# Optimization experiments

Hardware: AMD Instinct MI355X
Metric: run time of the kernel (lower is better)

## Reference

```python
import jax, jax.numpy as jnp
import numpy as np

V = 100000   # char_size
E = 256      # embedding_dim
H = 512      # hidden_dim
Hh = H // 2  # per-direction hidden
L = 20       # label_size
T = 4096     # sequence length
START = 18
STOP = 19
NEG = -10000.0


def setup_inputs() -> dict:
    key = jax.random.key(0)
    ks = jax.random.split(key, 16)
    s = 0.05
    x = jax.random.randint(ks[0], (1, T), 0, V, dtype=jnp.int32)
    emb = jax.random.normal(ks[1], (V, E), jnp.float32) * s
    w_ih_f = jax.random.normal(ks[2], (4 * Hh, E), jnp.float32) * s
    w_hh_f = jax.random.normal(ks[3], (4 * Hh, Hh), jnp.float32) * s
    b_ih_f = jax.random.normal(ks[4], (4 * Hh,), jnp.float32) * s
    b_hh_f = jax.random.normal(ks[5], (4 * Hh,), jnp.float32) * s
    w_ih_b = jax.random.normal(ks[6], (4 * Hh, E), jnp.float32) * s
    w_hh_b = jax.random.normal(ks[7], (4 * Hh, Hh), jnp.float32) * s
    b_ih_b = jax.random.normal(ks[8], (4 * Hh,), jnp.float32) * s
    b_hh_b = jax.random.normal(ks[9], (4 * Hh,), jnp.float32) * s
    w_out = jax.random.normal(ks[10], (L, H), jnp.float32) * s
    b_out = jax.random.normal(ks[11], (L,), jnp.float32) * s
    transitions = jax.random.normal(ks[12], (L, L), jnp.float32)
    transitions = transitions.at[START, :].set(NEG).at[:, STOP].set(NEG)
    h0 = jax.random.normal(ks[13], (2, Hh), jnp.float32)  # [direction, Hh], batch=1
    c0 = jax.random.normal(ks[14], (2, Hh), jnp.float32)
    return {"x": x, "emb": emb,
            "w_ih_f": w_ih_f, "w_hh_f": w_hh_f, "b_ih_f": b_ih_f, "b_hh_f": b_hh_f,
            "w_ih_b": w_ih_b, "w_hh_b": w_hh_b, "b_ih_b": b_ih_b, "b_hh_b": b_hh_b,
            "w_out": w_out, "b_out": b_out, "transitions": transitions,
            "h0": h0, "c0": c0}


def _lstm_dir(xs, w_ih, w_hh, b_ih, b_hh, h0, c0, reverse):
    # xs: [T, E]; PyTorch gate order i, f, g, o
    def step(carry, x_t):
        h, c = carry
        z = x_t @ w_ih.T + b_ih + h @ w_hh.T + b_hh  # [4*Hh]
        i, f, g, o = jnp.split(z, 4)
        i = jax.nn.sigmoid(i); f = jax.nn.sigmoid(f); o = jax.nn.sigmoid(o)
        g = jnp.tanh(g)
        c = f * c + i * g
        h = o * jnp.tanh(c)
        return (h, c), h
    _, hs = jax.lax.scan(step, (h0, c0), xs, reverse=reverse)
    return hs  # [T, Hh]


def _viterbi(feats, transitions):
    # feats: [T, L]; transitions[to, from]
    alpha0 = jnp.full((L,), NEG, feats.dtype).at[START].set(0.0)
    trT = transitions.T  # [from, to]
    def step(alpha, frame):
        smat = alpha[:, None] + frame[None, :] + trT  # [from, to]
        return jnp.max(smat, axis=0), jnp.argmax(smat, axis=0)
    alpha, bptrs = jax.lax.scan(step, alpha0, feats)  # bptrs: [T, L]
    final = alpha + transitions[STOP, :]
    score = jnp.max(final)
    best_last = jnp.argmax(final)
    def back(tag, bp):
        prev = bp[tag]
        return prev, prev
    _, prevs = jax.lax.scan(back, best_last, bptrs[1:], reverse=True)  # [T-1]
    path = jnp.concatenate([prevs, best_last[None]])  # [T]
    return score, path


def reference(x, emb, w_ih_f, w_hh_f, b_ih_f, b_hh_f, w_ih_b, w_hh_b, b_ih_b, b_hh_b,
              w_out, b_out, transitions, h0, c0):
    xs = emb[x[0]]  # [T, E], batch = 1
    h_f = _lstm_dir(xs, w_ih_f, w_hh_f, b_ih_f, b_hh_f, h0[0], c0[0], reverse=False)
    h_b = _lstm_dir(xs, w_ih_b, w_hh_b, b_ih_b, b_hh_b, h0[1], c0[1], reverse=True)
    lstm_out = jnp.concatenate([h_f, h_b], axis=-1)  # [T, H]
    feats = lstm_out @ w_out.T + b_out  # [T, L]
    score, path = _viterbi(feats, transitions)
    return score, path
```

## Files before the change

kernel.cpp:

```cpp
#include <hip/hip_runtime.h>
#include <hip/hip_bf16.h>
#include <stdint.h>

#define TT 4096
#define EE 256
#define LL 20
#define STARTT 18
#define STOPP 19
#define NEGV -10000.0f
#define NCH 256

typedef short v8s __attribute__((ext_vector_type(8)));
typedef float v4f __attribute__((ext_vector_type(4)));
typedef int   v4i __attribute__((ext_vector_type(4)));

__device__ inline float bf2f(unsigned short u){
  unsigned int x = ((unsigned int)u) << 16;
  return __builtin_bit_cast(float, x);
}
__device__ inline unsigned short f2bf(float f){
  unsigned int x = __builtin_bit_cast(unsigned int, f);
  unsigned int r = (x + 0x7FFFu + ((x >> 16) & 1u)) >> 16;
  return (unsigned short)r;
}

#if __has_builtin(__builtin_amdgcn_sdot4)
#define SDOT4(a,b,c) __builtin_amdgcn_sdot4((int)(a),(int)(b),(c),false)
#else
__device__ inline int sdot4_sw(int a, int b, int c){
  return c + (int)(char)(a)        * (int)(char)(b)
           + (int)(char)(a >> 8)   * (int)(char)(b >> 8)
           + (int)(char)(a >> 16)  * (int)(char)(b >> 16)
           + (int)(char)(a >> 24)  * (int)(char)(b >> 24);
}
#define SDOT4(a,b,c) sdot4_sw((int)(a),(int)(b),(c))
#endif

#define BARRIER_LDS() asm volatile("s_waitcnt lgkmcnt(0)\ns_barrier" ::: "memory")

constexpr size_t OFF_U    = 0;
constexpr size_t SZ_U     = 2ull*TT*1024*2;
constexpr size_t OFF_X    = OFF_U + SZ_U;
constexpr size_t SZ_X     = (size_t)TT*EE*2;
constexpr size_t OFF_WIH  = OFF_X + SZ_X;
constexpr size_t SZ_WIH   = 2048ull*256*2;
constexpr size_t OFF_BIAS = OFF_WIH + SZ_WIH;
constexpr size_t SZ_BIAS  = 2048ull*4;
constexpr size_t OFF_WQ   = OFF_BIAS + SZ_BIAS;
constexpr size_t SZ_WQ    = 2ull*8*8*4*64*16;
constexpr size_t OFF_WQD  = OFF_WQ + SZ_WQ;
constexpr size_t SZ_WQD   = 2ull*8*4*64*16;
constexpr size_t OFF_FS   = OFF_WQD + SZ_WQD;
constexpr size_t SZ_FS    = 2ull*256*16;
constexpr size_t OFF_WOP  = OFF_FS + SZ_FS;
constexpr size_t SZ_WOP   = 32ull*512*2;
constexpr size_t OFF_HOUT = OFF_WOP + SZ_WOP;
constexpr size_t SZ_HOUT  = (size_t)TT*512*2;
constexpr size_t OFF_FE   = OFF_HOUT + SZ_HOUT;
constexpr size_t SZ_FE    = (size_t)TT*LL*4;
constexpr size_t OFF_P    = OFF_FE + SZ_FE;
constexpr size_t SZ_P     = 256ull*400*4;
constexpr size_t OFF_BAL  = OFF_P + SZ_P;
constexpr size_t SZ_BAL   = 20736;
constexpr size_t OFF_BP   = OFF_BAL + SZ_BAL;
constexpr size_t SZ_BP    = (size_t)TT*LL;
constexpr size_t OFF_M    = OFF_BP + SZ_BP;
constexpr size_t SZ_M     = 256ull*LL;
constexpr size_t OFF_EG   = OFF_M + SZ_M + 64;


__global__ void k_gather(const int* __restrict__ x, const float* __restrict__ emb,
                         unsigned short* __restrict__ X){
  int t = blockIdx.x;
  int xt = x[t];
  const float4* src = (const float4*)(emb + (size_t)xt * EE);
  float4 v = src[threadIdx.x];
  ushort4 o;
  o.x = f2bf(v.x); o.y = f2bf(v.y); o.z = f2bf(v.z); o.w = f2bf(v.w);
  ((ushort4*)(X + (size_t)t * EE))[threadIdx.x] = o;
}

__global__ void k_wih(const float* __restrict__ wf, const float* __restrict__ wb,
                      unsigned short* __restrict__ WIH){
  int gid = blockIdx.x * 256 + threadIdx.x;
  int row = gid >> 5, c8 = gid & 31;
  const float* src = (row < 1024 ? wf + (size_t)row * EE : wb + (size_t)(row - 1024) * EE) + c8 * 8;
  unsigned short* dst = WIH + (size_t)row * 256 + c8 * 8;
#pragma unroll
  for (int i = 0; i < 8; i++) dst[i] = f2bf(src[i]);
}

__global__ void k_bias(const float* bf, const float* hf, const float* bb, const float* hb,
                       float* __restrict__ bias){
  int i = blockIdx.x * 256 + threadIdx.x;
  int r = i & 1023;
  bias[i] = (i < 1024) ? (bf[r] + hf[r]) : (bb[r] + hb[r]);
}

__global__ void k_wout(const float* __restrict__ wout, unsigned short* __restrict__ WOP){
  int gid = blockIdx.x * 256 + threadIdx.x;
  int row = gid >> 9, k = gid & 511;
  WOP[gid] = (row < LL) ? f2bf(wout[row * 512 + k]) : 0;
}

__global__ void k_whh9(const float* __restrict__ whf, const float* __restrict__ whb,
                       unsigned int* __restrict__ WQ, unsigned int* __restrict__ WQD,
                       float* __restrict__ FS){
  int row = blockIdx.x;
  int d = row >> 10, R = row & 1023;
  int g = R >> 8, J = R & 255;
  int w = J >> 5, tp = (J >> 4) & 1, n = J & 15;
  int nt = g * 2 + tp;
  const float* W = (d ? whb : whf) + (size_t)R * 256;
  int t = threadIdx.x;
  float4 v = ((const float4*)W)[t];
  float m = fmaxf(fmaxf(fabsf(v.x), fabsf(v.y)), fmaxf(fabsf(v.z), fabsf(v.w)));
#pragma unroll
  for (int o = 32; o >= 1; o >>= 1) m = fmaxf(m, __shfl_down(m, o));
  m = __shfl(m, 0);
  float sc = (m > 0.f) ? (m / 127.f) : 1.f;
  float inv = 1.f / sc;
  int a = (int)rintf(v.x * inv), b = (int)rintf(v.y * inv);
  int c = (int)rintf(v.z * inv), e4 = (int)rintf(v.w * inv);
  unsigned int pack = ((unsigned)a & 255u) | (((unsigned)b & 255u) << 8)
                    | (((unsigned)c & 255u) << 16) | (((unsigned)e4 & 255u) << 24);
  int kt = t >> 4, q = (t >> 2) & 3, comp = t & 3;
  int lane = q * 16 + n;
  if (nt == 7){
    size_t didx = (((size_t)d * 8 + w) * 4 + kt) * 64 + lane;
    WQD[didx * 4 + comp] = pack;
  } else {
    size_t widx = ((((size_t)d * 8 + w) * 8 + nt) * 4 + kt) * 64 + lane;
    WQ[widx * 4 + comp] = pack;
  }
  if (t == 0) FS[((size_t)d * 256 + J) * 4 + g] = sc;
}

__global__ void k_gemm_u(const unsigned short* __restrict__ X,
                         const unsigned short* __restrict__ WIH,
                         const float* __restrict__ bias,
                         unsigned short* __restrict__ U){
  int wave = threadIdx.x >> 6, l = threadIdx.x & 63;
  int tile = blockIdx.x * 4 + wave;
  int mt = tile & 255, nt = tile >> 8;
  int lm = l & 15, lq = l >> 4;
  const unsigned short* Arow = X   + (size_t)(mt * 16 + lm) * 256 + lq * 8;
  const unsigned short* Brow = WIH + (size_t)(nt * 16 + lm) * 256 + lq * 8;
  v4f acc = {0.f, 0.f, 0.f, 0.f};
#pragma unroll
  for (int kb = 0; kb < 8; kb++){
    v8s a = *(const v8s*)(Arow + kb * 32);
    v8s b = *(const v8s*)(Brow + kb * 32);
    acc = __builtin_amdgcn_mfma_f32_16x16x32_bf16(a, b, acc, 0, 0, 0);
  }
  int n = nt * 16 + lm;
  int dd = n >> 10, r = n & 1023;
  int g = r >> 8, J = r & 255;
  float bi = bias[n];
#pragma unroll
  for (int r4 = 0; r4 < 4; r4++){
    int t = mt * 16 + lq * 4 + r4;
    U[(((size_t)(dd * TT + t)) * 256 + J) * 4 + g] = f2bf(acc[r4] + bi);
  }
}


#define NT7(M) M(0) M(1) M(2) M(3) M(4) M(5) M(6)

#define DECLWB(nt) v4i wb0_##nt, wb1_##nt, wb2_##nt, wb3_##nt;
#define LOADWB(nt) { wb0_##nt = WQv[base + ((nt)*4 + 0) * 64]; \
                     wb1_##nt = WQv[base + ((nt)*4 + 1) * 64]; \
                     wb2_##nt = WQv[base + ((nt)*4 + 2) * 64]; \
                     wb3_##nt = WQv[base + ((nt)*4 + 3) * 64]; }
#define MF4(nt) \
  acc_##nt = __builtin_amdgcn_mfma_i32_16x16x64_i8(hA0, wb0_##nt, zero,     0, 0, 0); \
  acc_##nt = __builtin_amdgcn_mfma_i32_16x16x64_i8(hA1, wb1_##nt, acc_##nt, 0, 0, 0); \
  acc_##nt = __builtin_amdgcn_mfma_i32_16x16x64_i8(hA2, wb2_##nt, acc_##nt, 0, 0, 0); \
  acc_##nt = __builtin_amdgcn_mfma_i32_16x16x64_i8(hA3, wb3_##nt, acc_##nt, 0, 0, 0);

__global__ void __launch_bounds__(512)
__attribute__((amdgpu_waves_per_eu(2, 2)))
k_lstm13(
    const unsigned short* __restrict__ U, const v4i* __restrict__ WQv,
    const v4i* __restrict__ WQDv, const float4* __restrict__ FS4,
    const float* __restrict__ h0, const float* __restrict__ c0,
    unsigned short* __restrict__ hout){
  int d = blockIdx.x;
  int tid = threadIdx.x;
  int w = tid >> 6;
  int l = tid & 63;
  int q = l >> 4;
  int n = l & 15;
  int tp = l >> 5;
  int Jsel = w * 32 + tp * 16 + n;
  bool pub = ((l & 16) == 0);

  __shared__ __align__(16) unsigned char hb[2][256];

  NT7(DECLWB)
  v4i wd0, wd1, wd2, wd3;
  {
    size_t base = ((size_t)(d * 8 + w)) * 2048 + l;
    NT7(LOADWB)
    size_t dbase = ((size_t)(d * 8 + w)) * 256 + l;
    wd0 = WQDv[dbase];        wd1 = WQDv[dbase + 64];
    wd2 = WQDv[dbase + 128];  wd3 = WQDv[dbase + 192];
  }

  float4 fsv = FS4[(size_t)d * 256 + Jsel];
  float fs8x = fsv.x * (8.f/127.f), fs1x = fsv.x * (1.f/127.f);
  float fs8y = fsv.y * (8.f/127.f), fs1y = fsv.y * (1.f/127.f);
  float fs8z = fsv.z * (8.f/127.f), fs1z = fsv.z * (1.f/127.f);
  float fs8w = fsv.w * (8.f/127.f), fs1w = fsv.w * (1.f/127.f);

  float cst = c0[d * 256 + Jsel];
  if (pub){
    float hini = h0[d * 256 + Jsel];
    hini = fminf(fmaxf(hini, -8.f), 8.f);
    hb[0][Jsel] = (unsigned char)(char)(int)rintf(hini * (127.f / 8.f));
  }

  const unsigned short* Up0 = U + (size_t)d * TT * 1024 + (size_t)Jsel * 4;
  int stp = d ? -1 : 1;
  int tA = d ? TT - 1 : 0;
  uint2 u_c = *(const uint2*)(Up0 + (size_t)tA * 1024);
  uint2 u_n = *(const uint2*)(Up0 + (size_t)(tA + stp) * 1024);

  unsigned short* hp = hout + (size_t)tA * 512 + d * 256 + Jsel;

  v4i zero = {0, 0, 0, 0};

  __syncthreads();

  for (int s = 0; s < TT; s++){
    int par = s & 1;
    int tt = d ? (TT - 1 - s) : s;

    const char* hbase = (const char*)(&hb[par][0]) + (q << 4);
    v4i hA0 = *(const v4i*)(hbase);
    v4i hA1 = *(const v4i*)(hbase + 64);
    v4i hA2 = *(const v4i*)(hbase + 128);
    v4i hA3 = *(const v4i*)(hbase + 192);

    bool s0 = (s == 0);
    float fx = s0 ? fs8x : fs1x;
    float fy = s0 ? fs8y : fs1y;
    float fz = s0 ? fs8z : fs1z;
    float fw = s0 ? fs8w : fs1w;
    float u_i = bf2f((unsigned short)(u_c.x & 0xffffu));
    float u_f = bf2f((unsigned short)(u_c.x >> 16));
    float u_g = bf2f((unsigned short)(u_c.y & 0xffffu));
    float u_o = bf2f((unsigned short)(u_c.y >> 16));

    int ad = 0;
    ad = SDOT4(wd0.x, hA0.x, ad); ad = SDOT4(wd0.y, hA0.y, ad);
    ad = SDOT4(wd0.z, hA0.z, ad); ad = SDOT4(wd0.w, hA0.w, ad);
    ad = SDOT4(wd1.x, hA1.x, ad); ad = SDOT4(wd1.y, hA1.y, ad);
    ad = SDOT4(wd1.z, hA1.z, ad); ad = SDOT4(wd1.w, hA1.w, ad);
    ad = SDOT4(wd2.x, hA2.x, ad); ad = SDOT4(wd2.y, hA2.y, ad);
    ad = SDOT4(wd2.z, hA2.z, ad); ad = SDOT4(wd2.w, hA2.w, ad);
    ad = SDOT4(wd3.x, hA3.x, ad); ad = SDOT4(wd3.y, hA3.y, ad);
    ad = SDOT4(wd3.z, hA3.z, ad); ad = SDOT4(wd3.w, hA3.w, ad);
    ad += __shfl_xor(ad, 16);
    ad += __shfl_xor(ad, 32);

    v4i acc_0, acc_1, acc_2, acc_3, acc_4, acc_5, acc_6;
    MF4(0) MF4(1)
    int aI = tp ? acc_1[0] : acc_0[0];
    float zi = fmaf((float)aI, fx, u_i);
    float ea = __expf(-zi);
    float gi = __builtin_amdgcn_rcpf(1.f + ea);

    MF4(2) MF4(3)
    int aF = tp ? acc_3[0] : acc_2[0];
    float zf = fmaf((float)aF, fy, u_f);
    float eb = __expf(-zf);
    float gf = __builtin_amdgcn_rcpf(1.f + eb);

    MF4(4) MF4(5)
    int aG = tp ? acc_5[0] : acc_4[0];
    float zg = fmaf((float)aG, fz, u_g);
    float zc = fminf(fmaxf(zg, -20.f), 20.f);
    float ec = __expf(-2.f * zc);
    float gg = (1.f - ec) * __builtin_amdgcn_rcpf(1.f + ec);
    cst = fmaf(gf, cst, gi * gg);
    float cc = fminf(fmaxf(cst, -20.f), 20.f);
    float e2 = __expf(-2.f * cc);
    float th = (1.f - e2) * __builtin_amdgcn_rcpf(1.f + e2);

    MF4(6)
    int aO = tp ? ad : acc_6[0];
    float zo = fmaf((float)aO, fw, u_o);
    float ed = __expf(-zo);
    float go = __builtin_amdgcn_rcpf(1.f + ed);
    float h = go * th;

    u_c = u_n;
    {
      int t2 = tt + 2 * stp;
      t2 = t2 < 0 ? 0 : (t2 > TT - 1 ? TT - 1 : t2);
      u_n = *(const uint2*)(Up0 + (size_t)t2 * 1024);
    }

    if (pub){
      int qv = (int)rintf(h * 127.f);
      hb[par ^ 1][Jsel] = (unsigned char)(char)qv;
      *hp = f2bf(h);
    }
    hp += stp * 512;

    BARRIER_LDS();
  }
}

__global__ void k_feats2(const unsigned short* __restrict__ HOUT,
                         const unsigned short* __restrict__ WOP,
                         const float* __restrict__ bout,
                         float* __restrict__ feats){
  int wave = threadIdx.x >> 6, l = threadIdx.x & 63;
  int tile = blockIdx.x * 4 + wave;
  int mt = tile & 255, nt = tile >> 8;
  int lm = l & 15, lq = l >> 4;
  const unsigned short* Arow = HOUT + (size_t)(mt * 16 + lm) * 512 + lq * 8;
  const unsigned short* Brow = WOP  + (size_t)(nt * 16 + lm) * 512 + lq * 8;
  v4f acc = {0.f, 0.f, 0.f, 0.f};
#pragma unroll
  for (int kb = 0; kb < 16; kb++){
    v8s a = *(const v8s*)(Arow + kb * 32);
    v8s b = *(const v8s*)(Brow + kb * 32);
    acc = __builtin_amdgcn_mfma_f32_16x16x32_bf16(a, b, acc, 0, 0, 0);
  }
  int n = nt * 16 + lm;
  if (n < LL){
    float bi = bout[n];
#pragma unroll
    for (int r4 = 0; r4 < 4; r4++){
      int t = mt * 16 + lq * 4 + r4;
      feats[t * LL + n] = acc[r4] + bi;
    }
  }
}

__global__ void k_vchunk(const float* __restrict__ feats, const float* __restrict__ trans,
                         float* __restrict__ P){
  int c = blockIdx.x, j = threadIdx.x;
  __shared__ float Ps[2][LL][LL];
  bool act = j < LL;
  float trow[LL];
  if (act){
#pragma unroll
    for (int i = 0; i < LL; i++) trow[i] = trans[j * LL + i];
    for (int i = 0; i < LL; i++) Ps[0][i][j] = (i == j) ? 0.f : -1e30f;
  }
  __syncthreads();
  for (int s = 0; s < 16; s++){
    int t = c * 16 + s;
    int pb = s & 1;
    if (act){
      float fj = feats[t * LL + j];
      for (int i = 0; i < LL; i++){
        float m = Ps[pb][i][0] + trow[0];
#pragma unroll
        for (int mm = 1; mm < LL; mm++) m = fmaxf(m, Ps[pb][i][mm] + trow[mm]);
        Ps[pb ^ 1][i][j] = m + fj;
      }
    }
    __syncthreads();
  }
  if (act)
    for (int i = 0; i < LL; i++) P[((size_t)c * LL + i) * LL + j] = Ps[0][i][j];
}

__global__ void k_vscan(const float* __restrict__ P, float* __restrict__ bal){
  int tid = threadIdx.x;
  bool act = tid < LL;
  __shared__ float al[LL];
  __shared__ float Pl[400];
  if (act){
    float a = (tid == STARTT) ? 0.f : NEGV;
    al[tid] = a;
    bal[tid] = a;
  }
  for (int k = tid; k < 400; k += 64) Pl[k] = P[k];
  __syncthreads();
  for (int c = 0; c < NCH; c++){
    float p0 = 0.f, p1 = 0.f, p2 = 0.f, p3 = 0.f, p4 = 0.f, p5 = 0.f, p6 = 0.f;
    if (c + 1 < NCH){
      const float* Pn = P + (size_t)(c + 1) * 400;
      p0 = Pn[tid];        p1 = Pn[tid + 64];  p2 = Pn[tid + 128];
      p3 = Pn[tid + 192];  p4 = Pn[tid + 256]; p5 = Pn[tid + 320];
      if (tid + 384 < 400) p6 = Pn[tid + 384];
    }
    float m = -1e30f;
    if (act){
      m = al[0] + Pl[tid];
#pragma unroll
      for (int i = 1; i < LL; i++) m = fmaxf(m, al[i] + Pl[i * LL + tid]);
    }
    __syncthreads();
    if (act){
      al[tid] = m;
      bal[(c + 1) * LL + tid] = m;
    }
    if (c + 1 < NCH){
      Pl[tid] = p0;        Pl[tid + 64] = p1;  Pl[tid + 128] = p2;
      Pl[tid + 192] = p3;  Pl[tid + 256] = p4; Pl[tid + 320] = p5;
      if (tid + 384 < 400) Pl[tid + 384] = p6;
    }
    __syncthreads();
  }
}

__global__ void k_vbp(const float* __restrict__ feats, const float* __restrict__ trans,
                      const float* __restrict__ bal, unsigned char* __restrict__ bp,
                      unsigned char* __restrict__ M){
  int c = blockIdx.x, j = threadIdx.x;
  bool act = j < LL;
  __shared__ float al[2][LL];
  __shared__ unsigned char bpl[16][LL];
  float trow[LL];
  if (act){
#pragma unroll
    for (int i = 0; i < LL; i++) trow[i] = trans[j * LL + i];
    al[0][j] = bal[c * LL + j];
  }
  __syncthreads();
  for (int s = 0; s < 16; s++){
    int t = c * 16 + s;
    int pb = s & 1;
    if (act){
      float m = al[pb][0] + trow[0];
      int arg = 0;
#pragma unroll
      for (int i = 1; i < LL; i++){
        float v = al[pb][i] + trow[i];
        if (v > m){ m = v; arg = i; }
      }
      bpl[s][j] = (unsigned char)arg;
      bp[(size_t)t * LL + j] = (unsigned char)arg;
      al[pb ^ 1][j] = m + feats[t * LL + j];
    }
    __syncthreads();
  }
  if (act){
    int tag = j;
    for (int s = 15; s >= 0; s--) tag = bpl[s][tag];
    M[c * LL + j] = (unsigned char)tag;
  }
}

__global__ void k_vtag(const float* __restrict__ bal, const float* __restrict__ trans,
                       const unsigned char* __restrict__ M, int* __restrict__ Eg,
                       float* __restrict__ out){
  int tid = threadIdx.x;
  __shared__ unsigned char Ml[NCH * LL];
  __shared__ float fin[LL];
  for (int k = tid; k < NCH * LL; k += 64) Ml[k] = M[k];
  if (tid < LL) fin[tid] = bal[NCH * LL + tid] + trans[STOPP * LL + tid];
  __syncthreads();
  if (tid == 0){
    float m = fin[0]; int arg = 0;
    for (int i = 1; i < LL; i++) if (fin[i] > m){ m = fin[i]; arg = i; }
    out[0] = m;
    int tag = arg;
    Eg[NCH - 1] = tag;
    for (int c = NCH - 1; c >= 1; c--){
      tag = Ml[c * LL + tag];
      Eg[c - 1] = tag;
    }
  }
}

__global__ void k_vemit(const int* __restrict__ Eg, const unsigned char* __restrict__ bp,
                        float* __restrict__ out){
  int c = threadIdx.x;
  int tag = Eg[c];
  out[1 + c * 16 + 15] = (float)tag;
  for (int s = 15; s >= 1; s--){
    tag = bp[(size_t)(c * 16 + s) * LL + tag];
    out[1 + c * 16 + s - 1] = (float)tag;
  }
}

extern "C" void kernel_launch(void* const* d_in, const int* in_sizes, int n_in,
                              void* d_out, int out_size, void* d_ws, size_t ws_size,
                              hipStream_t stream){
  (void)in_sizes; (void)n_in; (void)out_size; (void)ws_size;
  const int*   x     = (const int*)d_in[0];
  const float* emb   = (const float*)d_in[1];
  const float* wihf  = (const float*)d_in[2];
  const float* whhf  = (const float*)d_in[3];
  const float* bihf  = (const float*)d_in[4];
  const float* bhhf  = (const float*)d_in[5];
  const float* wihb  = (const float*)d_in[6];
  const float* whhb  = (const float*)d_in[7];
  const float* bihb  = (const float*)d_in[8];
  const float* bhhb  = (const float*)d_in[9];
  const float* wout  = (const float*)d_in[10];
  const float* bout  = (const float*)d_in[11];
  const float* trans = (const float*)d_in[12];
  const float* h0    = (const float*)d_in[13];
  const float* c0    = (const float*)d_in[14];
  float* out = (float*)d_out;
  char* ws = (char*)d_ws;

  unsigned short* U    = (unsigned short*)(ws + OFF_U);
  unsigned short* X    = (unsigned short*)(ws + OFF_X);
  unsigned short* WIH  = (unsigned short*)(ws + OFF_WIH);
  float*          BIAS = (float*)(ws + OFF_BIAS);
  unsigned int*   WQ   = (unsigned int*)(ws + OFF_WQ);
  unsigned int*   WQD  = (unsigned int*)(ws + OFF_WQD);
  float*          FS   = (float*)(ws + OFF_FS);
  unsigned short* WOP  = (unsigned short*)(ws + OFF_WOP);
  unsigned short* HOUT = (unsigned short*)(ws + OFF_HOUT);
  float*          FE   = (float*)(ws + OFF_FE);
  float*          P    = (float*)(ws + OFF_P);
  float*          BAL  = (float*)(ws + OFF_BAL);
  unsigned char*  BP   = (unsigned char*)(ws + OFF_BP);
  unsigned char*  M    = (unsigned char*)(ws + OFF_M);
  int*            EG   = (int*)(ws + OFF_EG);

  k_gather<<<TT, 64, 0, stream>>>(x, emb, X);
  k_wih<<<256, 256, 0, stream>>>(wihf, wihb, WIH);
  k_bias<<<8, 256, 0, stream>>>(bihf, bhhf, bihb, bhhb, BIAS);
  k_wout<<<64, 256, 0, stream>>>(wout, WOP);
  k_whh9<<<2048, 64, 0, stream>>>(whhf, whhb, WQ, WQD, FS);
  k_gemm_u<<<8192, 256, 0, stream>>>(X, WIH, BIAS, U);
  k_lstm13<<<2, 512, 0, stream>>>(U, (const v4i*)WQ, (const v4i*)WQD,
                                  (const float4*)FS, h0, c0, HOUT);
  k_feats2<<<128, 256, 0, stream>>>(HOUT, WOP, bout, FE);
  k_vchunk<<<NCH, 64, 0, stream>>>(FE, trans, P);
  k_vscan<<<1, 64, 0, stream>>>(P, BAL);
  k_vbp<<<NCH, 64, 0, stream>>>(FE, trans, BAL, BP, M);
  k_vtag<<<1, 64, 0, stream>>>(BAL, trans, M, EG, out);
  k_vemit<<<1, 256, 0, stream>>>(EG, BP, out);
}
```

Measured before the change: 3.758 ms.

## Move two output-gate tiles to SDOT and interleave MFMA chains across tiles

The recurrent LSTM step now computes only six gate tiles with MFMA and handles both output-gate tiles (6 and 7) with VALU dot4 instructions, so the matrix unit and the vector unit work in parallel. The MFMA calls are reordered so each k-step is issued across all six independent accumulators, instead of four dependent MFMAs per tile. This is meant to hide MFMA dependency latency on the serial critical path. In exchange, all gate activations now wait until every MFMA has finished, and each step does twice as many dot4 instructions and holds more weight registers.

```diff
diff --git a/kernel.cpp b/kernel.cpp
--- a/kernel.cpp
+++ b/kernel.cpp
@@ -49,7 +49,7 @@
 constexpr size_t OFF_WQ   = OFF_BIAS + SZ_BIAS;
 constexpr size_t SZ_WQ    = 2ull*8*8*4*64*16;
 constexpr size_t OFF_WQD  = OFF_WQ + SZ_WQ;
-constexpr size_t SZ_WQD   = 2ull*8*4*64*16;
+constexpr size_t SZ_WQD   = 2ull*8*2*4*64*16;
 constexpr size_t OFF_FS   = OFF_WQD + SZ_WQD;
 constexpr size_t SZ_FS    = 2ull*256*16;
 constexpr size_t OFF_WOP  = OFF_FS + SZ_FS;
@@ -103,9 +103,9 @@
   WOP[gid] = (row < LL) ? f2bf(wout[row * 512 + k]) : 0;
 }
 
-__global__ void k_whh9(const float* __restrict__ whf, const float* __restrict__ whb,
-                       unsigned int* __restrict__ WQ, unsigned int* __restrict__ WQD,
-                       float* __restrict__ FS){
+__global__ void k_whh10(const float* __restrict__ whf, const float* __restrict__ whb,
+                        unsigned int* __restrict__ WQ, unsigned int* __restrict__ WQD,
+                        float* __restrict__ FS){
   int row = blockIdx.x;
   int d = row >> 10, R = row & 1023;
   int g = R >> 8, J = R & 255;
@@ -126,8 +126,8 @@
                     | (((unsigned)c & 255u) << 16) | (((unsigned)e4 & 255u) << 24);
   int kt = t >> 4, q = (t >> 2) & 3, comp = t & 3;
   int lane = q * 16 + n;
-  if (nt == 7){
-    size_t didx = (((size_t)d * 8 + w) * 4 + kt) * 64 + lane;
+  if (nt >= 6){
+    size_t didx = (((size_t)(d * 8 + w) * 2 + (nt - 6)) * 4 + kt) * 64 + lane;
     WQD[didx * 4 + comp] = pack;
   } else {
     size_t widx = ((((size_t)d * 8 + w) * 8 + nt) * 4 + kt) * 64 + lane;
@@ -165,22 +165,22 @@
 }
 
 
-#define NT7(M) M(0) M(1) M(2) M(3) M(4) M(5) M(6)
+#define NT6(M) M(0) M(1) M(2) M(3) M(4) M(5)
 
 #define DECLWB(nt) v4i wb0_##nt, wb1_##nt, wb2_##nt, wb3_##nt;
 #define LOADWB(nt) { wb0_##nt = WQv[base + ((nt)*4 + 0) * 64]; \
                      wb1_##nt = WQv[base + ((nt)*4 + 1) * 64]; \
                      wb2_##nt = WQv[base + ((nt)*4 + 2) * 64]; \
                      wb3_##nt = WQv[base + ((nt)*4 + 3) * 64]; }
-#define MF4(nt) \
-  acc_##nt = __builtin_amdgcn_mfma_i32_16x16x64_i8(hA0, wb0_##nt, zero,     0, 0, 0); \
-  acc_##nt = __builtin_amdgcn_mfma_i32_16x16x64_i8(hA1, wb1_##nt, acc_##nt, 0, 0, 0); \
-  acc_##nt = __builtin_amdgcn_mfma_i32_16x16x64_i8(hA2, wb2_##nt, acc_##nt, 0, 0, 0); \
-  acc_##nt = __builtin_amdgcn_mfma_i32_16x16x64_i8(hA3, wb3_##nt, acc_##nt, 0, 0, 0);
+#define DECLACC(nt) v4i acc_##nt;
+#define MFA(nt) acc_##nt = __builtin_amdgcn_mfma_i32_16x16x64_i8(hA0, wb0_##nt, zero,     0, 0, 0);
+#define MFB(nt) acc_##nt = __builtin_amdgcn_mfma_i32_16x16x64_i8(hA1, wb1_##nt, acc_##nt, 0, 0, 0);
+#define MFC(nt) acc_##nt = __builtin_amdgcn_mfma_i32_16x16x64_i8(hA2, wb2_##nt, acc_##nt, 0, 0, 0);
+#define MFD(nt) acc_##nt = __builtin_amdgcn_mfma_i32_16x16x64_i8(hA3, wb3_##nt, acc_##nt, 0, 0, 0);
 
 __global__ void __launch_bounds__(512)
 __attribute__((amdgpu_waves_per_eu(2, 2)))
-k_lstm13(
+k_lstm14(
     const unsigned short* __restrict__ U, const v4i* __restrict__ WQv,
     const v4i* __restrict__ WQDv, const float4* __restrict__ FS4,
     const float* __restrict__ h0, const float* __restrict__ c0,
@@ -197,14 +197,17 @@
 
   __shared__ __align__(16) unsigned char hb[2][256];
 
-  NT7(DECLWB)
-  v4i wd0, wd1, wd2, wd3;
+  NT6(DECLWB)
+  v4i w6_0, w6_1, w6_2, w6_3;
+  v4i w7_0, w7_1, w7_2, w7_3;
   {
     size_t base = ((size_t)(d * 8 + w)) * 2048 + l;
-    NT7(LOADWB)
-    size_t dbase = ((size_t)(d * 8 + w)) * 256 + l;
-    wd0 = WQDv[dbase];        wd1 = WQDv[dbase + 64];
-    wd2 = WQDv[dbase + 128];  wd3 = WQDv[dbase + 192];
+    NT6(LOADWB)
+    size_t dbase = ((size_t)(d * 8 + w)) * 512 + l;
+    w6_0 = WQDv[dbase];        w6_1 = WQDv[dbase + 64];
+    w6_2 = WQDv[dbase + 128];  w6_3 = WQDv[dbase + 192];
+    w7_0 = WQDv[dbase + 256];  w7_1 = WQDv[dbase + 320];
+    w7_2 = WQDv[dbase + 384];  w7_3 = WQDv[dbase + 448];
   }
 
   float4 fsv = FS4[(size_t)d * 256 + Jsel];
@@ -241,6 +244,30 @@
     v4i hA1 = *(const v4i*)(hbase + 64);
     v4i hA2 = *(const v4i*)(hbase + 128);
     v4i hA3 = *(const v4i*)(hbase + 192);
+
+    NT6(DECLACC)
+    NT6(MFA)
+    NT6(MFB)
+    NT6(MFC)
+    NT6(MFD)
+
+    int a6 = 0, a7 = 0;
+    a6 = SDOT4(w6_0.x, hA0.x, a6); a7 = SDOT4(w7_0.x, hA0.x, a7);
+    a6 = SDOT4(w6_0.y, hA0.y, a6); a7 = SDOT4(w7_0.y, hA0.y, a7);
+    a6 = SDOT4(w6_0.z, hA0.z, a6); a7 = SDOT4(w7_0.z, hA0.z, a7);
+    a6 = SDOT4(w6_0.w, hA0.w, a6); a7 = SDOT4(w7_0.w, hA0.w, a7);
+    a6 = SDOT4(w6_1.x, hA1.x, a6); a7 = SDOT4(w7_1.x, hA1.x, a7);
+    a6 = SDOT4(w6_1.y, hA1.y, a6); a7 = SDOT4(w7_1.y, hA1.y, a7);
+    a6 = SDOT4(w6_1.z, hA1.z, a6); a7 = SDOT4(w7_1.z, hA1.z, a7);
+    a6 = SDOT4(w6_1.w, hA1.w, a6); a7 = SDOT4(w7_1.w, hA1.w, a7);
+    a6 = SDOT4(w6_2.x, hA2.x, a6); a7 = SDOT4(w7_2.x, hA2.x, a7);
+    a6 = SDOT4(w6_2.y, hA2.y, a6); a7 = SDOT4(w7_2.y, hA2.y, a7);
+    a6 = SDOT4(w6_2.z, hA2.z, a6); a7 = SDOT4(w7_2.z, hA2.z, a7);
+    a6 = SDOT4(w6_2.w, hA2.w, a6); a7 = SDOT4(w7_2.w, hA2.w, a7);
+    a6 = SDOT4(w6_3.x, hA3.x, a6); a7 = SDOT4(w7_3.x, hA3.x, a7);
+    a6 = SDOT4(w6_3.y, hA3.y, a6); a7 = SDOT4(w7_3.y, hA3.y, a7);
+    a6 = SDOT4(w6_3.z, hA3.z, a6); a7 = SDOT4(w7_3.z, hA3.z, a7);
+    a6 = SDOT4(w6_3.w, hA3.w, a6); a7 = SDOT4(w7_3.w, hA3.w, a7);
 
     bool s0 = (s == 0);
     float fx = s0 ? fs8x : fs1x;
@@ -252,55 +279,41 @@
     float u_g = bf2f((unsigned short)(u_c.y & 0xffffu));
     float u_o = bf2f((unsigned short)(u_c.y >> 16));
 
-    int ad = 0;
-    ad = SDOT4(wd0.x, hA0.x, ad); ad = SDOT4(wd0.y, hA0.y, ad);
-    ad = SDOT4(wd0.z, hA0.z, ad); ad = SDOT4(wd0.w, hA0.w, ad);
-    ad = SDOT4(wd1.x, hA1.x, ad); ad = SDOT4(wd1.y, hA1.y, ad);
-    ad = SDOT4(wd1.z, hA1.z, ad); ad = SDOT4(wd1.w, hA1.w, ad);
-    ad = SDOT4(wd2.x, hA2.x, ad); ad = SDOT4(wd2.y, hA2.y, ad);
-    ad = SDOT4(wd2.z, hA2.z, ad); ad = SDOT4(wd2.w, hA2.w, ad);
-    ad = SDOT4(wd3.x, hA3.x, ad); ad = SDOT4(wd3.y, hA3.y, ad);
-    ad = SDOT4(wd3.z, hA3.z, ad); ad = SDOT4(wd3.w, hA3.w, ad);
-    ad += __shfl_xor(ad, 16);
-    ad += __shfl_xor(ad, 32);
-
-    v4i acc_0, acc_1, acc_2, acc_3, acc_4, acc_5, acc_6;
-    MF4(0) MF4(1)
-    int aI = tp ? acc_1[0] : acc_0[0];
-    float zi = fmaf((float)aI, fx, u_i);
-    float ea = __expf(-zi);
-    float gi = __builtin_amdgcn_rcpf(1.f + ea);
-
-    MF4(2) MF4(3)
-    int aF = tp ? acc_3[0] : acc_2[0];
-    float zf = fmaf((float)aF, fy, u_f);
-    float eb = __expf(-zf);
-    float gf = __builtin_amdgcn_rcpf(1.f + eb);
-
-    MF4(4) MF4(5)
-    int aG = tp ? acc_5[0] : acc_4[0];
-    float zg = fmaf((float)aG, fz, u_g);
-    float zc = fminf(fmaxf(zg, -20.f), 20.f);
-    float ec = __expf(-2.f * zc);
-    float gg = (1.f - ec) * __builtin_amdgcn_rcpf(1.f + ec);
-    cst = fmaf(gf, cst, gi * gg);
-    float cc = fminf(fmaxf(cst, -20.f), 20.f);
-    float e2 = __expf(-2.f * cc);
-    float th = (1.f - e2) * __builtin_amdgcn_rcpf(1.f + e2);
-
-    MF4(6)
-    int aO = tp ? ad : acc_6[0];
-    float zo = fmaf((float)aO, fw, u_o);
-    float ed = __expf(-zo);
-    float go = __builtin_amdgcn_rcpf(1.f + ed);
-    float h = go * th;
-
     u_c = u_n;
     {
       int t2 = tt + 2 * stp;
       t2 = t2 < 0 ? 0 : (t2 > TT - 1 ? TT - 1 : t2);
       u_n = *(const uint2*)(Up0 + (size_t)t2 * 1024);
     }
+
+    a6 += __shfl_xor(a6, 16);  a7 += __shfl_xor(a7, 16);
+    a6 += __shfl_xor(a6, 32);  a7 += __shfl_xor(a7, 32);
+
+    int aI = tp ? acc_1[0] : acc_0[0];
+    int aF = tp ? acc_3[0] : acc_2[0];
+    int aG = tp ? acc_5[0] : acc_4[0];
+    int aO = tp ? a7 : a6;
+
+    float zi = fmaf((float)aI, fx, u_i);
+    float zf = fmaf((float)aF, fy, u_f);
+    float zg = fmaf((float)aG, fz, u_g);
+    float zo = fmaf((float)aO, fw, u_o);
+
+    float ea = __expf(-zi);
+    float gi = __builtin_amdgcn_rcpf(1.f + ea);
+    float eb = __expf(-zf);
+    float gf = __builtin_amdgcn_rcpf(1.f + eb);
+    float zc = fminf(fmaxf(zg, -20.f), 20.f);
+    float ec = __expf(-2.f * zc);
+    float gg = (1.f - ec) * __builtin_amdgcn_rcpf(1.f + ec);
+    float ed = __expf(-zo);
+    float go = __builtin_amdgcn_rcpf(1.f + ed);
+
+    cst = fmaf(gf, cst, gi * gg);
+    float cc = fminf(fmaxf(cst, -20.f), 20.f);
+    float e2 = __expf(-2.f * cc);
+    float th = (1.f - e2) * __builtin_amdgcn_rcpf(1.f + e2);
+    float h = go * th;
 
     if (pub){
       int qv = (int)rintf(h * 127.f);
@@ -524,9 +537,9 @@
   k_wih<<<256, 256, 0, stream>>>(wihf, wihb, WIH);
   k_bias<<<8, 256, 0, stream>>>(bihf, bhhf, bihb, bhhb, BIAS);
   k_wout<<<64, 256, 0, stream>>>(wout, WOP);
-  k_whh9<<<2048, 64, 0, stream>>>(whhf, whhb, WQ, WQD, FS);
+  k_whh10<<<2048, 64, 0, stream>>>(whhf, whhb, WQ, WQD, FS);
   k_gemm_u<<<8192, 256, 0, stream>>>(X, WIH, BIAS, U);
-  k_lstm13<<<2, 512, 0, stream>>>(U, (const v4i*)WQ, (const v4i*)WQD,
+  k_lstm14<<<2, 512, 0, stream>>>(U, (const v4i*)WQ, (const v4i*)WQD,
                                   (const float4*)FS, h0, c0, HOUT);
   k_feats2<<<128, 256, 0, stream>>>(HOUT, WOP, bout, FE);
   k_vchunk<<<NCH, 64, 0, stream>>>(FE, trans, P);
```

After: 4.192 ms. +11.5%, slower.
